# Kernel optimization log

Hardware: AMD Instinct MI355X
Metric: run time of the kernel (lower is better)

Reference implementation:

```python
import jax, jax.numpy as jnp
import numpy as np

B, L, C = 8, 4096, 256
H = 8            # num_heads
D = C // H       # head_dim = 32
CHUNK = 128


def _build_slopes(n):
    # ALiBi slopes for power-of-2 n: 2^(-8/n * (i+1)); cast fp16 like the torch module
    s = np.array([2.0 ** (-(8.0 / n) * (i + 1)) for i in range(n)], dtype=np.float32)
    return jnp.asarray(s.astype(np.float16).astype(np.float32))  # [H]


def setup_inputs() -> dict:
    key = jax.random.key(0)
    ks = jax.random.split(key, 6)
    x = jax.random.normal(ks[0], (B, L, C), dtype=jnp.float32)
    rel_pos = jax.random.normal(ks[1], (1, L, C), dtype=jnp.float32) * 0.02  # trunc_normal std=0.02
    qkv_w = jax.random.normal(ks[2], (3 * C, C), dtype=jnp.float32) * (C ** -0.5)
    q_gamma = jnp.ones((H, 1, D), dtype=jnp.float32) / (D ** 0.5)
    k_gamma = jnp.ones((H, 1, D), dtype=jnp.float32) / (D ** 0.5)
    proj_w = jax.random.normal(ks[3], (C, C), dtype=jnp.float32) * (C ** -0.5)
    proj_b = jnp.zeros((C,), dtype=jnp.float32)
    return {"x": x, "rel_pos": rel_pos, "qkv_w": qkv_w, "q_gamma": q_gamma,
            "k_gamma": k_gamma, "proj_w": proj_w, "proj_b": proj_b}


def _rms_norm(t, gamma):
    # t: [B,H,L,D]; gamma: [H,1,D]. F.normalize(dim=-1) then * sqrt(D) * gamma
    n = jnp.sqrt(jnp.sum(t * t, axis=-1, keepdims=True))
    t = t / jnp.maximum(n, 1e-12)
    return t * (D ** 0.5) * gamma[None]


def _lightning_attn(q, k, v, slopes):
    # q,k,v: [B,H,L,D]; slopes: [H]. o_t = sum_{s<=t} exp(-slope*(t-s)) (q_t.k_s) v_s
    nc = L // CHUNK
    c = CHUNK
    qc = q.reshape(B, H, nc, c, D)
    kc = k.reshape(B, H, nc, c, D)
    vc = v.reshape(B, H, nc, c, D)

    idx = jnp.arange(c, dtype=jnp.float32)
    diff = idx[:, None] - idx[None, :]                       # [c,c]
    s = slopes[:, None, None]                                # [H,1,1]
    mask = jnp.where(diff >= 0, jnp.exp(-s * diff), 0.0)     # [H,c,c]

    # intra-chunk: [B,H,nc,c,c]
    scores = jnp.einsum("bhncd,bhnmd->bhncm", qc, kc) * mask[None, :, None]
    o_intra = jnp.einsum("bhncm,bhnmd->bhncd", scores, vc)

    # inter-chunk recurrence over decayed KV state [B,H,D,D]
    q_decay = jnp.exp(-slopes[:, None] * idx[None, :])[None, :, :, None]        # [1,H,c,1]
    k_decay = jnp.exp(-slopes[:, None] * (c - idx[None, :]))[None, :, :, None]  # [1,H,c,1]
    blk_decay = jnp.exp(-slopes * c)[:, None, None]                             # [H,1,1]

    def step(kv, inp):
        qi, ki, vi = inp                                   # each [B,H,c,D]
        o = jnp.einsum("bhcd,bhde->bhce", qi * q_decay, kv)
        kv = blk_decay * kv + jnp.einsum("bhcd,bhce->bhde", ki * k_decay, vi)
        return kv, o

    kv0 = jnp.zeros((B, H, D, D), dtype=q.dtype)
    qs = jnp.moveaxis(qc, 2, 0)  # [nc,B,H,c,D]
    ks_ = jnp.moveaxis(kc, 2, 0)
    vs = jnp.moveaxis(vc, 2, 0)
    _, o_inter = jax.lax.scan(step, kv0, (qs, ks_, vs))    # [nc,B,H,c,D]
    o_inter = jnp.moveaxis(o_inter, 0, 2)                  # [B,H,nc,c,D]

    return (o_intra + o_inter).reshape(B, H, L, D)


def reference(x, rel_pos, qkv_w, q_gamma, k_gamma, proj_w, proj_b):
    slopes = _build_slopes(H)
    h = x + rel_pos                                        # [B,L,C]
    qkv = h @ qkv_w.T                                      # [B,L,3C]
    qkv = qkv.reshape(B, L, 3, H, D).transpose(2, 0, 3, 1, 4)  # [3,B,H,L,D]
    q, k, v = qkv[0], qkv[1], qkv[2]
    q = q * (D ** -0.5)            # no-op through normalize, kept for fidelity
    q = _rms_norm(q, q_gamma)
    k = _rms_norm(k, k_gamma)
    o = _lightning_attn(q, k, v, slopes)                   # [B,H,L,D]
    o = o.transpose(0, 2, 1, 3).reshape(B, L, C)
    return o @ proj_w.T + proj_b
```

## Files before the change

### kernel.cpp

```cpp
#include <hip/hip_runtime.h>
#include <hip/hip_bf16.h>

#define B_ 8
#define L_ 4096
#define C_ 256
#define H_ 8
#define D_ 32
#define CHUNK_ 128
#define NC_ 32
#define M_ (B_*L_)

typedef _Float16 f16x8 __attribute__((ext_vector_type(8)));
typedef _Float16 f16x4 __attribute__((ext_vector_type(4)));
typedef float    f32x4 __attribute__((ext_vector_type(4)));

#define GLOAD_LDS16(g, l) __builtin_amdgcn_global_load_lds( \
    (const __attribute__((address_space(1))) unsigned int*)(g), \
    (__attribute__((address_space(3))) unsigned int*)(l), 16, 0, 0)

__global__ __launch_bounds__(256) void k_prep(
    const float* __restrict__ x, const float* __restrict__ rel,
    const float* __restrict__ qw, const float* __restrict__ pw,
    _Float16* __restrict__ h, _Float16* __restrict__ qwb, _Float16* __restrict__ pwb)
{
    const int bx = blockIdx.x;
    if (bx < 4096) {
        const int i = (bx * 256 + threadIdx.x) * 8;
        float4 x0 = *(const float4*)(x + i);
        float4 x1 = *(const float4*)(x + i + 4);
        const int ri = i & (L_ * C_ - 1);
        float4 r0 = *(const float4*)(rel + ri);
        float4 r1 = *(const float4*)(rel + ri + 4);
        f16x8 o = { (_Float16)(x0.x + r0.x), (_Float16)(x0.y + r0.y),
                    (_Float16)(x0.z + r0.z), (_Float16)(x0.w + r0.w),
                    (_Float16)(x1.x + r1.x), (_Float16)(x1.y + r1.y),
                    (_Float16)(x1.z + r1.z), (_Float16)(x1.w + r1.w) };
        *(f16x8*)(h + i) = o;
    } else {
        const int i = ((bx - 4096) * 256 + threadIdx.x) * 4;
        const float* src; _Float16* dst; int off;
        if (i < 768 * 256) { src = qw; dst = qwb; off = i; }
        else               { src = pw; dst = pwb; off = i - 768 * 256; }
        float4 v = *(const float4*)(src + off);
        f16x4 o = { (_Float16)v.x, (_Float16)v.y, (_Float16)v.z, (_Float16)v.w };
        *(f16x4*)(dst + off) = o;
    }
}

__global__ __launch_bounds__(256) void k_qkv_gemm(
    const _Float16* __restrict__ A, const _Float16* __restrict__ Bw,
    const float* __restrict__ qg, const float* __restrict__ kg,
    _Float16* __restrict__ Qg, _Float16* __restrict__ Kg, _Float16* __restrict__ Vtg)
{
    __shared__ __align__(16) char smem[34816];
    _Float16* As = (_Float16*)smem;
    _Float16* Bs = As + 128 * 32;
    _Float16* Ws = (_Float16*)smem;

    const int blk = blockIdx.x;
    const int xcd = blk & 7;
    const int t   = blk >> 3;
    const int by  = xcd * 32 + (t & 31);
    const int bx  = t >> 5;
    const int m0 = by * 128;
    const int n0 = bx * 128;

    const int tid = threadIdx.x;
    const int wv = tid >> 6, ln = tid & 63;
    const int lr = ln >> 2, lc = (ln & 3) * 8;
    const int wm = (wv >> 1) * 64, wn = (wv & 1) * 64;
    const int fr = ln & 15, fk = (ln >> 4) * 8;

    f32x4 acc[4][4] = {};
    const _Float16* ga = A  + (size_t)(m0 + wv * 16 + lr) * 256 + lc;
    const _Float16* gb = Bw + (size_t)(n0 + wv * 16 + lr) * 256 + lc;

    for (int k0 = 0; k0 < 256; k0 += 32) {
        GLOAD_LDS16(ga + k0,            As + (wv * 16) * 32);
        GLOAD_LDS16(ga + k0 + 64 * 256, As + (64 + wv * 16) * 32);
        GLOAD_LDS16(gb + k0,            Bs + (wv * 16) * 32);
        GLOAD_LDS16(gb + k0 + 64 * 256, Bs + (64 + wv * 16) * 32);
        __syncthreads();
        f16x8 af[4], bf[4];
#pragma unroll
        for (int i = 0; i < 4; ++i)
            af[i] = *(const f16x8*)(As + (wm + i * 16 + fr) * 32 + fk);
#pragma unroll
        for (int j = 0; j < 4; ++j)
            bf[j] = *(const f16x8*)(Bs + (wn + j * 16 + fr) * 32 + fk);
#pragma unroll
        for (int i = 0; i < 4; ++i)
#pragma unroll
            for (int j = 0; j < 4; ++j)
                acc[i][j] = __builtin_amdgcn_mfma_f32_16x16x32_f16(
                    af[i], bf[j], acc[i][j], 0, 0, 0);
        __syncthreads();
    }

    const int cr = (ln >> 4) * 4, cc = ln & 15;
    const int kind = n0 >> 8;
    const int col0 = (n0 & 255) + wn;
    const int bb = m0 >> 12, l00 = m0 & 4095;
    const int hbase = (n0 & 255) >> 5;

    if (kind < 2) {
        const float* gsrc = kind ? kg : qg;
        float gma[2][2];
#pragma unroll
        for (int jp = 0; jp < 2; ++jp)
#pragma unroll
            for (int jj = 0; jj < 2; ++jj)
                gma[jp][jj] = gsrc[((col0 >> 5) + jp) * 32 + jj * 16 + cc];
#pragma unroll
        for (int i = 0; i < 4; ++i)
#pragma unroll
            for (int r = 0; r < 4; ++r) {
                const int irow = wm + i * 16 + cr + r;
#pragma unroll
                for (int jp = 0; jp < 2; ++jp) {
                    const float a0 = acc[i][jp * 2][r];
                    const float a1 = acc[i][jp * 2 + 1][r];
                    float ss = a0 * a0 + a1 * a1;
                    ss += __shfl_xor(ss, 1);
                    ss += __shfl_xor(ss, 2);
                    ss += __shfl_xor(ss, 4);
                    ss += __shfl_xor(ss, 8);
                    const float sc = 5.656854249492381f / fmaxf(sqrtf(ss), 1e-12f);
                    Ws[irow * 136 + wn + jp * 32 + cc]      = (_Float16)(a0 * sc * gma[jp][0]);
                    Ws[irow * 136 + wn + jp * 32 + 16 + cc] = (_Float16)(a1 * sc * gma[jp][1]);
                }
            }
        __syncthreads();
        _Float16* P = kind ? Kg : Qg;
#pragma unroll
        for (int kk = 0; kk < 8; ++kk) {
            const int c = kk * 256 + tid;
            const int hh = c >> 9;
            const int rr = (c >> 2) & 127;
            const int part = (c & 3) * 8;
            f16x8 v8 = *(const f16x8*)(Ws + rr * 136 + hh * 32 + part);
            *(f16x8*)(P + ((size_t)(bb * 8 + hbase + hh) * 4096 + l00 + rr) * 32 + part) = v8;
        }
    } else {
#pragma unroll
        for (int i = 0; i < 4; ++i)
#pragma unroll
            for (int j = 0; j < 4; ++j) {
                const int colL = wn + j * 16 + cc;
                const int row0 = wm + i * 16 + cr;
                f16x4 v4 = { (_Float16)acc[i][j][0], (_Float16)acc[i][j][1],
                             (_Float16)acc[i][j][2], (_Float16)acc[i][j][3] };
                *(f16x4*)(Ws + colL * 132 + row0) = v4;
            }
        __syncthreads();
#pragma unroll
        for (int kk = 0; kk < 8; ++kk) {
            const int q = kk * 256 + tid;
            const int c = q >> 4;
            const int seg = q & 15;
            const int col = (n0 & 255) + c;
            const int hh = col >> 5, e = col & 31;
            f16x8 v8 = *(const f16x8*)(Ws + c * 132 + seg * 8);
            *(f16x8*)(Vtg + ((size_t)(bb * 8 + hh) * 32 + e) * 4096 + l00 + seg * 8) = v8;
        }
    }
}

__global__ __launch_bounds__(64) void k_chunk_kv(
    const _Float16* __restrict__ Kg, const _Float16* __restrict__ Vtg,
    float* __restrict__ kvbuf)
{
    __shared__ _Float16 Vp[32 * 136];
    __shared__ _Float16 Kp[32 * 136];
    const int blk = blockIdx.x;
    const int n  = blk & 31;
    const int bh = blk >> 5;
    const int h  = bh & 7;
    const float sl2 = exp2f(-(float)(h + 1)) * 1.44269504f;
    const int ln = threadIdx.x;
    const _Float16* Kc = Kg  + ((size_t)bh * 4096 + n * CHUNK_) * 32;
    const _Float16* Vc = Vtg + (size_t)bh * 32 * 4096 + n * CHUNK_;
#pragma unroll
    for (int i = 0; i < 8; ++i) {
        const int flat = i * 64 + ln;
        const int e = flat >> 4, seg = flat & 15;
        f16x8 v8 = *(const f16x8*)(Vc + (size_t)e * 4096 + seg * 8);
        *(f16x8*)(Vp + e * 136 + seg * 8) = v8;
        const int pos = flat >> 2, d0 = (flat & 3) * 8;
        f16x8 k8 = *(const f16x8*)(Kc + flat * 8);
#pragma unroll
        for (int j = 0; j < 8; ++j) Kp[(d0 + j) * 136 + pos] = k8[j];
    }
    __syncthreads();
    const int fr = ln & 15, fk = (ln >> 4) * 8;
    const float r = exp2f(sl2);
    float rj[8];
    rj[0] = 1.f;
#pragma unroll
    for (int j = 1; j < 8; ++j) rj[j] = rj[j - 1] * r;
    f32x4 acc[2][2] = {};
    for (int k0 = 0; k0 < 128; k0 += 32) {
        const float e0 = exp2f(-sl2 * (float)(CHUNK_ - (k0 + fk)));
        f16x8 av[2], bd[2];
#pragma unroll
        for (int i = 0; i < 2; ++i)
            av[i] = *(const f16x8*)(Vp + (i * 16 + fr) * 136 + k0 + fk);
#pragma unroll
        for (int jt = 0; jt < 2; ++jt) {
            f16x8 kraw = *(const f16x8*)(Kp + (jt * 16 + fr) * 136 + k0 + fk);
            f16x8 kb;
#pragma unroll
            for (int j = 0; j < 8; ++j)
                kb[j] = (_Float16)((float)kraw[j] * (e0 * rj[j]));
            bd[jt] = kb;
        }
#pragma unroll
        for (int i = 0; i < 2; ++i)
#pragma unroll
            for (int jt = 0; jt < 2; ++jt)
                acc[i][jt] = __builtin_amdgcn_mfma_f32_16x16x32_f16(
                    av[i], bd[jt], acc[i][jt], 0, 0, 0);
    }
    const int cr = (ln >> 4) * 4, cc = ln & 15;
    float* outp = kvbuf + (size_t)blk * 1024;
#pragma unroll
    for (int i = 0; i < 2; ++i)
#pragma unroll
        for (int jt = 0; jt < 2; ++jt)
#pragma unroll
            for (int rr = 0; rr < 4; ++rr)
                outp[(i * 16 + cr + rr) * 32 + jt * 16 + cc] = acc[i][jt][rr];
}

__global__ __launch_bounds__(256) void k_scan(float* __restrict__ kvbuf)
{
    const int bh = blockIdx.x;
    const int tid = threadIdx.x;
    const float slope = exp2f(-(float)((bh & 7) + 1));
    const float bd = __expf(-slope * (float)CHUNK_);
    float4 st = {0.f, 0.f, 0.f, 0.f};
    float4* base = (float4*)(kvbuf + (size_t)bh * NC_ * 1024) + tid;
#pragma unroll
    for (int g = 0; g < 4; ++g) {
        float4 tmp[8];
#pragma unroll
        for (int k = 0; k < 8; ++k) tmp[k] = base[(g * 8 + k) * 256];
#pragma unroll
        for (int k = 0; k < 8; ++k) {
            base[(g * 8 + k) * 256] = st;
            st.x = bd * st.x + tmp[k].x;
            st.y = bd * st.y + tmp[k].y;
            st.z = bd * st.z + tmp[k].z;
            st.w = bd * st.w + tmp[k].w;
        }
    }
}

__global__ __launch_bounds__(256) void k_attn(
    const _Float16* __restrict__ Qg, const _Float16* __restrict__ Kg,
    const _Float16* __restrict__ Vtg, const float* __restrict__ kvbuf,
    _Float16* __restrict__ attnp)
{
    __shared__ __align__(16) _Float16 Ss[128 * 136];
    __shared__ __align__(16) _Float16 KVt[32 * 40];
    __shared__ float ejs[CHUNK_];
    _Float16* Os = Ss;
    const int blk = blockIdx.x;
    const int n  = blk & 31;
    const int bh = blk >> 5;
    const int h  = bh & 7;
    const float sl2 = exp2f(-(float)(h + 1)) * 1.44269504f;
    const int tid = threadIdx.x;
    const int wv = tid >> 6, ln = tid & 63;
    const int fr = ln & 15, fk = (ln >> 4) * 8;
    const int cr = (ln >> 4) * 4, cc = ln & 15;

    const _Float16* Qc = Qg + ((size_t)bh * 4096 + n * CHUNK_) * 32;
    const _Float16* Kc = Kg + ((size_t)bh * 4096 + n * CHUNK_) * 32;
    const _Float16* Vc = Vtg + (size_t)bh * 32 * 4096 + n * CHUNK_;

    {
        const float* kvp = kvbuf + (size_t)blk * 1024;
        f32x4 kv4f = *(const f32x4*)(kvp + tid * 4);
        f16x4 kv4 = { (_Float16)kv4f[0], (_Float16)kv4f[1],
                      (_Float16)kv4f[2], (_Float16)kv4f[3] };
        *(f16x4*)(KVt + (tid >> 3) * 40 + (tid & 7) * 4) = kv4;
    }
    if (tid < CHUNK_) ejs[tid] = exp2f(sl2 * (float)tid);
    __syncthreads();

    f16x8 aq[2];
#pragma unroll
    for (int i = 0; i < 2; ++i)
        aq[i] = *(const f16x8*)(Qc + (wv * 32 + i * 16 + fr) * 32 + fk);

    f32x4 sacc[2][8] = {};
#pragma unroll
    for (int j = 0; j < 8; ++j) {
        f16x8 bk = *(const f16x8*)(Kc + (j * 16 + fr) * 32 + fk);
#pragma unroll
        for (int i = 0; i < 2; ++i)
            sacc[i][j] = __builtin_amdgcn_mfma_f32_16x16x32_f16(aq[i], bk, sacc[i][j], 0, 0, 0);
    }
    f32x4 iacc[2][2] = {};
#pragma unroll
    for (int ct = 0; ct < 2; ++ct) {
        f16x8 bkv = *(const f16x8*)(KVt + (ct * 16 + fr) * 40 + fk);
#pragma unroll
        for (int i = 0; i < 2; ++i)
            iacc[i][ct] = __builtin_amdgcn_mfma_f32_16x16x32_f16(aq[i], bkv, iacc[i][ct], 0, 0, 0);
    }
    float ejr[8];
#pragma unroll
    for (int j = 0; j < 8; ++j) ejr[j] = ejs[j * 16 + cc];
    const float c1 = exp2f(-sl2);
    float qd_save[2][4];
#pragma unroll
    for (int i = 0; i < 2; ++i) {
        float er = exp2f(-sl2 * (float)(wv * 32 + i * 16 + cr));
#pragma unroll
        for (int r = 0; r < 4; ++r) {
            const int irow = wv * 32 + i * 16 + cr + r;
            qd_save[i][r] = er;
#pragma unroll
            for (int j = 0; j < 8; ++j) {
                const int jcol = j * 16 + cc;
                const float w = (jcol <= irow) ? ejr[j] * er : 0.f;
                Ss[irow * 136 + jcol] = (_Float16)(sacc[i][j][r] * w);
            }
            er *= c1;
        }
    }
    __syncthreads();

    f32x4 oacc[2][2] = {};
#pragma unroll
    for (int k = 0; k < 4; ++k) {
        f16x8 as[2], bv[2];
#pragma unroll
        for (int i = 0; i < 2; ++i)
            as[i] = *(const f16x8*)(Ss + (wv * 32 + i * 16 + fr) * 136 + k * 32 + fk);
#pragma unroll
        for (int ct = 0; ct < 2; ++ct)
            bv[ct] = *(const f16x8*)(Vc + (size_t)(ct * 16 + fr) * 4096 + k * 32 + fk);
#pragma unroll
        for (int i = 0; i < 2; ++i)
#pragma unroll
            for (int ct = 0; ct < 2; ++ct)
                oacc[i][ct] = __builtin_amdgcn_mfma_f32_16x16x32_f16(as[i], bv[ct], oacc[i][ct], 0, 0, 0);
    }
    __syncthreads();
#pragma unroll
    for (int i = 0; i < 2; ++i)
#pragma unroll
        for (int r = 0; r < 4; ++r) {
            const int irow = wv * 32 + i * 16 + cr + r;
            const float qd = qd_save[i][r];
            Os[irow * 40 + cc]      = (_Float16)(oacc[i][0][r] + qd * iacc[i][0][r]);
            Os[irow * 40 + 16 + cc] = (_Float16)(oacc[i][1][r] + qd * iacc[i][1][r]);
        }
    __syncthreads();
    _Float16* abase = attnp + ((size_t)bh * 4096 + n * CHUNK_) * 32;
#pragma unroll
    for (int kk = 0; kk < 2; ++kk) {
        const int c = kk * 256 + tid;
        const int rr = c >> 2;
        const int part = (c & 3) * 8;
        *(f16x8*)(abase + rr * 32 + part) = *(const f16x8*)(Os + rr * 40 + part);
    }
}

__global__ __launch_bounds__(256) void k_proj_gemm(
    const _Float16* __restrict__ attnp, const _Float16* __restrict__ Bw,
    const float* __restrict__ bias, float* __restrict__ Cc)
{
    __shared__ _Float16 As[128 * 32];
    __shared__ _Float16 Bs[128 * 32];
    const int blk = blockIdx.x;
    const int xcd = blk & 7;
    const int t   = blk >> 3;
    const int m0 = (xcd * 32 + (t & 31)) * 128;
    const int n0 = (t >> 5) * 128;

    const int tid = threadIdx.x;
    const int wv = tid >> 6, ln = tid & 63;
    const int lr = ln >> 2;
    const int lc = (ln & 3) * 8;
    const int wm = (wv >> 1) * 64;
    const int wn = (wv & 1) * 64;
    const int fr = ln & 15;
    const int fk = (ln >> 4) * 8;

    f32x4 acc[4][4] = {};
    const int gmrow = m0 + wv * 16 + lr;
    const _Float16* ga = attnp +
        ((size_t)(gmrow >> 12) * 8 * 4096 + (gmrow & 4095)) * 32 + lc;
    const _Float16* gb = Bw + (size_t)(n0 + wv * 16 + lr) * 256 + lc;

    for (int k0 = 0; k0 < 256; k0 += 32) {
        const size_t hoff = (size_t)(k0 >> 5) * (4096 * 32);
        GLOAD_LDS16(ga + hoff,           As + (wv * 16) * 32);
        GLOAD_LDS16(ga + hoff + 64 * 32, As + (64 + wv * 16) * 32);
        GLOAD_LDS16(gb + k0,             Bs + (wv * 16) * 32);
        GLOAD_LDS16(gb + k0 + 64 * 256,  Bs + (64 + wv * 16) * 32);
        __syncthreads();
        f16x8 af[4], bf[4];
#pragma unroll
        for (int i = 0; i < 4; ++i)
            af[i] = *(const f16x8*)(As + (wm + i * 16 + fr) * 32 + fk);
#pragma unroll
        for (int j = 0; j < 4; ++j)
            bf[j] = *(const f16x8*)(Bs + (wn + j * 16 + fr) * 32 + fk);
#pragma unroll
        for (int i = 0; i < 4; ++i)
#pragma unroll
            for (int j = 0; j < 4; ++j)
                acc[i][j] = __builtin_amdgcn_mfma_f32_16x16x32_f16(
                    af[i], bf[j], acc[i][j], 0, 0, 0);
        __syncthreads();
    }
    const int cr = (ln >> 4) * 4;
    const int cc = ln & 15;
#pragma unroll
    for (int i = 0; i < 4; ++i)
#pragma unroll
        for (int j = 0; j < 4; ++j) {
            const int row = m0 + wm + i * 16 + cr;
            const int col = n0 + wn + j * 16 + cc;
            float* cp = Cc + (size_t)row * 256 + col;
            const float bb = bias[col];
#pragma unroll
            for (int r = 0; r < 4; ++r) cp[(size_t)r * 256] = acc[i][j][r] + bb;
        }
}

extern "C" void kernel_launch(void* const* d_in, const int* in_sizes, int n_in,
                              void* d_out, int out_size, void* d_ws, size_t ws_size,
                              hipStream_t stream)
{
    const float* x     = (const float*)d_in[0];
    const float* rel   = (const float*)d_in[1];
    const float* qkv_w = (const float*)d_in[2];
    const float* qg    = (const float*)d_in[3];
    const float* kg    = (const float*)d_in[4];
    const float* pw    = (const float*)d_in[5];
    const float* pb    = (const float*)d_in[6];
    float* out = (float*)d_out;
    char* wsb = (char*)d_ws;

    float*    kvb   = (float*)wsb;
    _Float16* Qg    = (_Float16*)(wsb + ((size_t)8  << 20));
    _Float16* Kg    = (_Float16*)(wsb + ((size_t)24 << 20));
    _Float16* Vtg   = (_Float16*)(wsb + ((size_t)40 << 20));
    _Float16* attnp = (_Float16*)(wsb + ((size_t)56 << 20));
    _Float16* hb    = (_Float16*)(wsb + ((size_t)72 << 20));
    _Float16* qwb   = (_Float16*)(wsb + ((size_t)88 << 20));
    _Float16* pwb   = (_Float16*)(wsb + ((size_t)89 << 20));

    k_prep<<<4352, 256, 0, stream>>>(x, rel, qkv_w, pw, hb, qwb, pwb);
    k_qkv_gemm<<<1536, 256, 0, stream>>>(hb, qwb, qg, kg, Qg, Kg, Vtg);
    k_chunk_kv<<<2048, 64, 0, stream>>>(Kg, Vtg, kvb);
    k_scan<<<64, 256, 0, stream>>>(kvb);
    k_attn<<<2048, 256, 0, stream>>>(Qg, Kg, Vtg, kvb, attnp);
    k_proj_gemm<<<512, 256, 0, stream>>>(attnp, pwb, pb, out);
}
```

Measured before the change: 168.5 us.

## Skip masked causal tiles in chunk attention and drop block barriers

The attention kernel now has each wave compute only the score tiles and score·V steps that lie on or below the causal diagonal for its rows. It reads the inter-chunk KV state straight from global memory instead of staging it in LDS, and computes the decay factors in registers. Because every wave then works only on its own rows, all __syncthreads are removed. The scan kernel is split into four 64-thread blocks per head, giving more blocks for the serial recurrence. The risk is extra divergence and redundant KV loads per wave in exchange for fewer MFMAs and barriers.

```diff
diff --git a/kernel.cpp b/kernel.cpp
--- a/kernel.cpp
+++ b/kernel.cpp
@@ -232,14 +232,16 @@
                 outp[(i * 16 + cr + rr) * 32 + jt * 16 + cc] = acc[i][jt][rr];
 }
 
-__global__ __launch_bounds__(256) void k_scan(float* __restrict__ kvbuf)
-{
-    const int bh = blockIdx.x;
+__global__ __launch_bounds__(64) void k_scan(float* __restrict__ kvbuf)
+{
+    const int blk = blockIdx.x;
+    const int bh  = blk >> 2;
+    const int grp = blk & 3;
     const int tid = threadIdx.x;
     const float slope = exp2f(-(float)((bh & 7) + 1));
     const float bd = __expf(-slope * (float)CHUNK_);
     float4 st = {0.f, 0.f, 0.f, 0.f};
-    float4* base = (float4*)(kvbuf + (size_t)bh * NC_ * 1024) + tid;
+    float4* base = (float4*)(kvbuf + (size_t)bh * NC_ * 1024) + grp * 64 + tid;
 #pragma unroll
     for (int g = 0; g < 4; ++g) {
         float4 tmp[8];
@@ -262,9 +264,7 @@
     _Float16* __restrict__ attnp)
 {
     __shared__ __align__(16) _Float16 Ss[128 * 136];
-    __shared__ __align__(16) _Float16 KVt[32 * 40];
-    __shared__ float ejs[CHUNK_];
-    _Float16* Os = Ss;
+    __shared__ __align__(16) _Float16 Os[128 * 40];
     const int blk = blockIdx.x;
     const int n  = blk & 31;
     const int bh = blk >> 5;
@@ -274,46 +274,49 @@
     const int wv = tid >> 6, ln = tid & 63;
     const int fr = ln & 15, fk = (ln >> 4) * 8;
     const int cr = (ln >> 4) * 4, cc = ln & 15;
+    const int jmax = 2 * wv + 2;
 
     const _Float16* Qc = Qg + ((size_t)bh * 4096 + n * CHUNK_) * 32;
     const _Float16* Kc = Kg + ((size_t)bh * 4096 + n * CHUNK_) * 32;
     const _Float16* Vc = Vtg + (size_t)bh * 32 * 4096 + n * CHUNK_;
-
-    {
-        const float* kvp = kvbuf + (size_t)blk * 1024;
-        f32x4 kv4f = *(const f32x4*)(kvp + tid * 4);
-        f16x4 kv4 = { (_Float16)kv4f[0], (_Float16)kv4f[1],
-                      (_Float16)kv4f[2], (_Float16)kv4f[3] };
-        *(f16x4*)(KVt + (tid >> 3) * 40 + (tid & 7) * 4) = kv4;
-    }
-    if (tid < CHUNK_) ejs[tid] = exp2f(sl2 * (float)tid);
-    __syncthreads();
+    const float* kvp = kvbuf + (size_t)blk * 1024;
 
     f16x8 aq[2];
 #pragma unroll
     for (int i = 0; i < 2; ++i)
         aq[i] = *(const f16x8*)(Qc + (wv * 32 + i * 16 + fr) * 32 + fk);
 
-    f32x4 sacc[2][8] = {};
-#pragma unroll
-    for (int j = 0; j < 8; ++j) {
-        f16x8 bk = *(const f16x8*)(Kc + (j * 16 + fr) * 32 + fk);
-#pragma unroll
-        for (int i = 0; i < 2; ++i)
-            sacc[i][j] = __builtin_amdgcn_mfma_f32_16x16x32_f16(aq[i], bk, sacc[i][j], 0, 0, 0);
-    }
     f32x4 iacc[2][2] = {};
 #pragma unroll
     for (int ct = 0; ct < 2; ++ct) {
-        f16x8 bkv = *(const f16x8*)(KVt + (ct * 16 + fr) * 40 + fk);
+        const float* kp = kvp + (ct * 16 + fr) * 32 + fk;
+        f32x4 k0 = *(const f32x4*)kp;
+        f32x4 k1 = *(const f32x4*)(kp + 4);
+        f16x8 bkv = { (_Float16)k0[0], (_Float16)k0[1], (_Float16)k0[2], (_Float16)k0[3],
+                      (_Float16)k1[0], (_Float16)k1[1], (_Float16)k1[2], (_Float16)k1[3] };
 #pragma unroll
         for (int i = 0; i < 2; ++i)
             iacc[i][ct] = __builtin_amdgcn_mfma_f32_16x16x32_f16(aq[i], bkv, iacc[i][ct], 0, 0, 0);
     }
+
+    f32x4 sacc[2][8];
+#pragma unroll
+    for (int j = 0; j < 8; ++j) {
+        if (j >= jmax) continue;
+        f16x8 bk = *(const f16x8*)(Kc + (j * 16 + fr) * 32 + fk);
+#pragma unroll
+        for (int i = 0; i < 2; ++i) {
+            f32x4 z = {};
+            sacc[i][j] = __builtin_amdgcn_mfma_f32_16x16x32_f16(aq[i], bk, z, 0, 0, 0);
+        }
+    }
+
+    const float c1  = exp2f(-sl2);
+    const float r16 = exp2f(sl2 * 16.f);
     float ejr[8];
-#pragma unroll
-    for (int j = 0; j < 8; ++j) ejr[j] = ejs[j * 16 + cc];
-    const float c1 = exp2f(-sl2);
+    ejr[0] = exp2f(sl2 * (float)cc);
+#pragma unroll
+    for (int j = 1; j < 8; ++j) ejr[j] = ejr[j - 1] * r16;
     float qd_save[2][4];
 #pragma unroll
     for (int i = 0; i < 2; ++i) {
@@ -324,6 +327,7 @@
             qd_save[i][r] = er;
 #pragma unroll
             for (int j = 0; j < 8; ++j) {
+                if (j >= jmax) continue;
                 const int jcol = j * 16 + cc;
                 const float w = (jcol <= irow) ? ejr[j] * er : 0.f;
                 Ss[irow * 136 + jcol] = (_Float16)(sacc[i][j][r] * w);
@@ -331,11 +335,11 @@
             er *= c1;
         }
     }
-    __syncthreads();
 
     f32x4 oacc[2][2] = {};
 #pragma unroll
     for (int k = 0; k < 4; ++k) {
+        if (k > wv) continue;
         f16x8 as[2], bv[2];
 #pragma unroll
         for (int i = 0; i < 2; ++i)
@@ -349,7 +353,7 @@
             for (int ct = 0; ct < 2; ++ct)
                 oacc[i][ct] = __builtin_amdgcn_mfma_f32_16x16x32_f16(as[i], bv[ct], oacc[i][ct], 0, 0, 0);
     }
-    __syncthreads();
+
 #pragma unroll
     for (int i = 0; i < 2; ++i)
 #pragma unroll
@@ -359,14 +363,15 @@
             Os[irow * 40 + cc]      = (_Float16)(oacc[i][0][r] + qd * iacc[i][0][r]);
             Os[irow * 40 + 16 + cc] = (_Float16)(oacc[i][1][r] + qd * iacc[i][1][r]);
         }
-    __syncthreads();
     _Float16* abase = attnp + ((size_t)bh * 4096 + n * CHUNK_) * 32;
 #pragma unroll
-    for (int kk = 0; kk < 2; ++kk) {
-        const int c = kk * 256 + tid;
-        const int rr = c >> 2;
+    for (int u = 0; u < 2; ++u) {
+        const int c = ln * 2 + u;
+        const int rloc = c >> 2;
         const int part = (c & 3) * 8;
-        *(f16x8*)(abase + rr * 32 + part) = *(const f16x8*)(Os + rr * 40 + part);
+        const int irow = wv * 32 + rloc;
+        f16x8 v8 = *(const f16x8*)(Os + irow * 40 + part);
+        *(f16x8*)(abase + irow * 32 + part) = v8;
     }
 }
 
@@ -460,7 +465,7 @@
     k_prep<<<4352, 256, 0, stream>>>(x, rel, qkv_w, pw, hb, qwb, pwb);
     k_qkv_gemm<<<1536, 256, 0, stream>>>(hb, qwb, qg, kg, Qg, Kg, Vtg);
     k_chunk_kv<<<2048, 64, 0, stream>>>(Kg, Vtg, kvb);
-    k_scan<<<64, 256, 0, stream>>>(kvb);
+    k_scan<<<256, 64, 0, stream>>>(kvb);
     k_attn<<<2048, 256, 0, stream>>>(Qg, Kg, Vtg, kvb, attnp);
     k_proj_gemm<<<512, 256, 0, stream>>>(attnp, pwb, pb, out);
 }
```

Result: slower. 177.9 us (+5.6%).
